# Kernel tuning notes

Hardware: AMD Instinct MI355X
Metric: run time of the kernel (lower is better)

Reference implementation:

```python
import jax, jax.numpy as jnp
import numpy as np

B, L, D = 4, 2048, 1024
H, DK, DV = 16, 64, 64


def setup_inputs() -> dict:
    key = jax.random.key(0)
    ks = jax.random.split(key, 11)
    s = 1.0 / np.sqrt(D)
    so = 1.0 / np.sqrt(H * DV)
    return {
        "query": jax.random.normal(ks[0], (B, L, D), jnp.float32),
        "key": jax.random.normal(ks[1], (B, L, D), jnp.float32),
        "value": jax.random.normal(ks[2], (B, L, D), jnp.float32),
        "W_q": jax.random.uniform(ks[3], (D, H * DK), jnp.float32, -s, s),
        "b_q": jax.random.uniform(ks[4], (H * DK,), jnp.float32, -s, s),
        "W_k": jax.random.uniform(ks[5], (D, H * DK), jnp.float32, -s, s),
        "b_k": jax.random.uniform(ks[6], (H * DK,), jnp.float32, -s, s),
        "W_v": jax.random.uniform(ks[7], (D, H * DV), jnp.float32, -s, s),
        "b_v": jax.random.uniform(ks[8], (H * DV,), jnp.float32, -s, s),
        "W_o": jax.random.uniform(ks[9], (H * DV, D), jnp.float32, -so, so),
        "b_o": jax.random.uniform(ks[10], (D,), jnp.float32, -so, so),
    }


def reference(query, key, value, W_q, b_q, W_k, b_k, W_v, b_v, W_o, b_o):
    # QKV projections, then split heads: [B, L, H*d] -> [B, H, L, d]
    q = (query @ W_q + b_q).reshape(B, L, H, DK).transpose(0, 2, 1, 3)
    k = (key @ W_k + b_k).reshape(B, L, H, DK).transpose(0, 2, 1, 3)
    v = (value @ W_v + b_v).reshape(B, L, H, DV).transpose(0, 2, 1, 3)
    # scaled dot-product attention: softmax(q k^T / sqrt(dk)) v
    scores = jnp.einsum("bhqd,bhkd->bhqk", q, k) / jnp.sqrt(jnp.float32(DK))
    attn = jax.nn.softmax(scores, axis=-1)
    ctx = jnp.einsum("bhqk,bhkd->bhqd", attn, v)
    # combine heads: [B, H, L, dv] -> [B, L, H*dv], output projection
    out = ctx.transpose(0, 2, 1, 3).reshape(B, L, H * DV) @ W_o + b_o
    return out
```

## Files before the change

kernel.cpp:

```cpp
#include <hip/hip_runtime.h>

#define BATCH 4
#define LSEQ 2048
#define DMODEL 1024
#define NHEAD 16
#define DHEAD 64
#define MTOT (BATCH * LSEQ)

typedef _Float16 f16;
typedef _Float16 f16x8 __attribute__((ext_vector_type(8)));
typedef _Float16 f16x4 __attribute__((ext_vector_type(4)));
typedef _Float16 f16x2 __attribute__((ext_vector_type(2)));
typedef float f32x4 __attribute__((ext_vector_type(4)));
typedef float f32x16 __attribute__((ext_vector_type(16)));
typedef unsigned int u32;
typedef unsigned int u32x4 __attribute__((ext_vector_type(4)));

#define SCORE_SCALE 0.180336878f

typedef const __attribute__((address_space(1))) void gvoid;
typedef __attribute__((address_space(3))) void lvoid;
#define GLDS16(g, l) __builtin_amdgcn_global_load_lds((gvoid*)(g), (lvoid*)(l), 16, 0, 0)

#define WAITCNT(s) do { asm volatile("s_waitcnt " s ::: "memory"); \
                        __builtin_amdgcn_sched_barrier(0); } while (0)
#define BAR() __builtin_amdgcn_s_barrier()
#define SCHED0() __builtin_amdgcn_sched_barrier(0)

__global__ __launch_bounds__(256)
void cvt3_f32_f16(const float* __restrict__ in0, const float* __restrict__ in1,
                  const float* __restrict__ in2, f16* __restrict__ out, int n8)
{
    const int y = blockIdx.y;
    const float* in = (y == 0) ? in0 : (y == 1) ? in1 : in2;
    f16* o = out + (size_t)y * (size_t)n8 * 8;
    int i = blockIdx.x * 256 + threadIdx.x;
    if (i >= n8) return;
    float4 a = ((const float4*)in)[2 * i];
    float4 b = ((const float4*)in)[2 * i + 1];
    f16x8 v;
    v[0] = (f16)a.x; v[1] = (f16)a.y; v[2] = (f16)a.z; v[3] = (f16)a.w;
    v[4] = (f16)b.x; v[5] = (f16)b.y; v[6] = (f16)b.z; v[7] = (f16)b.w;
    ((f16x8*)o)[i] = v;
}

__global__ __launch_bounds__(256)
void wconv4(const float* __restrict__ W0, const float* __restrict__ W1,
            const float* __restrict__ W2, const float* __restrict__ W3,
            f16* __restrict__ WtBase)
{
    __shared__ float T[64][68];
    const int z = blockIdx.z;
    const float* W = (z == 0) ? W0 : (z == 1) ? W1 : (z == 2) ? W2 : W3;
    f16* Wt = WtBase + (size_t)z * DMODEL * DMODEL;
    const int t = threadIdx.x;
    const int k0 = blockIdx.y * 64, n0 = blockIdx.x * 64;
    const int tr = t >> 4, tc = (t & 15) * 4;
#pragma unroll
    for (int p = 0; p < 64; p += 16) {
        float4 v = *(const float4*)&W[(size_t)(k0 + tr + p) * DMODEL + n0 + tc];
        *(float4*)&T[tr + p][tc] = v;
    }
    __syncthreads();
    const int n = t >> 2, kc = (t & 3) * 16;
    f16x8 o0, o1;
#pragma unroll
    for (int j = 0; j < 8; ++j) o0[j] = (f16)T[kc + j][n];
#pragma unroll
    for (int j = 0; j < 8; ++j) o1[j] = (f16)T[kc + 8 + j][n];
    *(f16x8*)&Wt[(size_t)(n0 + n) * DMODEL + k0 + kc] = o0;
    *(f16x8*)&Wt[(size_t)(n0 + n) * DMODEL + k0 + kc + 8] = o1;
}

__global__ __launch_bounds__(512, 2)
void gemm_qkv(const f16* __restrict__ A, const f16* __restrict__ Bt,
              const float* __restrict__ b0, const float* __restrict__ b1,
              const float* __restrict__ b2, f16* __restrict__ Cout)
{
    __shared__ f16 As[2][2][128][64];
    __shared__ f16 Bs[2][2][128][64];

    const int t = threadIdx.x;
    const int lane = t & 63;
    const int w = t >> 6, wr = w >> 2, wc = w & 3;
    const int quad = lane >> 4, m16 = lane & 15;
    const int m0 = blockIdx.x * 256, n0 = blockIdx.y * 256;
    const int which = n0 >> 10;

    const int sr = t >> 3;
    const int sc = ((t & 7) << 4) ^ ((sr & 7) << 4);
    const f16* Asrc = A + (size_t)which * MTOT * DMODEL
                        + (size_t)(m0 + sr) * DMODEL + (sc >> 1);
    const f16* Bsrc = Bt + (size_t)(n0 + sr) * DMODEL + (sc >> 1);

    auto stA = [&](int buf, int h, int kt) {
        const f16* s = Asrc + (size_t)(h * 128) * DMODEL + kt * 64;
        GLDS16(s,               &As[buf][h][0][0] + t * 8);
        GLDS16(s + 64 * DMODEL, &As[buf][h][64][0] + t * 8);
    };
    auto stB = [&](int buf, int h, int kt) {
        const f16* s = Bsrc + (size_t)(h * 128) * DMODEL + kt * 64;
        GLDS16(s,               &Bs[buf][h][0][0] + t * 8);
        GLDS16(s + 64 * DMODEL, &Bs[buf][h][64][0] + t * 8);
    };
    auto stageTile = [&](int k) {
        const int b = k & 1;
        stA(b, 0, k); stA(b, 1, k); stB(b, 0, k); stB(b, 1, k);
    };

    const int fsw = (m16 & 7) << 4;
    auto rdA = [&](int buf, int mf, int ks) -> f16x8 {
        return *(const f16x8*)((const char*)&As[buf][wr][0][0]
                               + (mf * 16 + m16) * 128
                               + ((ks * 64 + quad * 16) ^ fsw));
    };
    auto rdB = [&](int buf, int nf, int ks) -> f16x8 {
        return *(const f16x8*)((const char*)&Bs[buf][wc >> 1][0][0]
                               + ((wc & 1) * 64 + nf * 16 + m16) * 128
                               + ((ks * 64 + quad * 16) ^ fsw));
    };

    f32x4 acc[8][4] = {};

    auto compute = [&](int buf) {
        f16x8 af[4][2], bf[4][2];
#pragma unroll
        for (int nf = 0; nf < 4; ++nf)
#pragma unroll
            for (int ks = 0; ks < 2; ++ks)
                bf[nf][ks] = rdB(buf, nf, ks);
#pragma unroll
        for (int mg = 0; mg < 2; ++mg) {
#pragma unroll
            for (int mi = 0; mi < 4; ++mi)
#pragma unroll
                for (int ks = 0; ks < 2; ++ks)
                    af[mi][ks] = rdA(buf, mg * 4 + mi, ks);
#pragma unroll
            for (int mi = 0; mi < 4; ++mi)
#pragma unroll
                for (int ni = 0; ni < 4; ++ni)
#pragma unroll
                    for (int ks = 0; ks < 2; ++ks)
                        acc[mg * 4 + mi][ni] =
                            __builtin_amdgcn_mfma_f32_16x16x32_f16(
                                af[mi][ks], bf[ni][ks],
                                acc[mg * 4 + mi][ni], 0, 0, 0);
        }
    };

    const int NKT = DMODEL / 64;
    stageTile(0);
    stageTile(1);

#pragma unroll 2
    for (int k = 0; k < NKT - 2; ++k) {
        WAITCNT("vmcnt(8)");
        BAR(); SCHED0();
        compute(k & 1);
        WAITCNT("lgkmcnt(0)");
        BAR(); SCHED0();
        stageTile(k + 2);
        SCHED0();
    }
    WAITCNT("vmcnt(8)");
    BAR(); SCHED0();
    compute((NKT - 2) & 1);
    WAITCNT("lgkmcnt(0)");
    BAR(); SCHED0();
    WAITCNT("vmcnt(0)");
    BAR(); SCHED0();
    compute((NKT - 1) & 1);

    const float* bp = (which == 0) ? b0 : (which == 1) ? b1 : b2;
    const float scale = (which == 0) ? SCORE_SCALE : 1.0f;
    f16* o = Cout + (size_t)which * MTOT * DMODEL;
    float bv[4];
    int hh[4], dd[4];
#pragma unroll
    for (int nf = 0; nf < 4; ++nf) {
        const int nn = (n0 + wc * 64 + nf * 16 + m16) & 1023;
        bv[nf] = bp[nn];
        hh[nf] = nn >> 6;
        dd[nf] = nn & 63;
    }
#pragma unroll
    for (int mf = 0; mf < 8; ++mf) {
        const int mrow = m0 + wr * 128 + mf * 16 + quad * 4;
        const int b = mrow >> 11, l0 = mrow & (LSEQ - 1);
        if (which < 2) {
#pragma unroll
            for (int j = 0; j < 4; ++j)
#pragma unroll
                for (int nf = 0; nf < 4; ++nf) {
                    const float v = (acc[mf][nf][j] + bv[nf]) * scale;
                    o[(((size_t)(b * NHEAD + hh[nf]) * LSEQ + l0 + j) << 6)
                      + dd[nf]] = (f16)v;
                }
        } else {
#pragma unroll
            for (int nf = 0; nf < 4; ++nf) {
                f16x4 pk;
#pragma unroll
                for (int j = 0; j < 4; ++j) pk[j] = (f16)(acc[mf][nf][j] + bv[nf]);
                *(f16x4*)&o[(((size_t)(b * NHEAD + hh[nf]) << 6) + dd[nf]) * LSEQ
                            + l0] = pk;
            }
        }
    }
}

__global__ __launch_bounds__(256)
void gemm_f16(const f16* __restrict__ A, const f16* __restrict__ Bt,
              const float* __restrict__ b0, const float* __restrict__ b1,
              const float* __restrict__ b2, void* __restrict__ Cout, int fused)
{
    __shared__ f16 As2[2][128][32];
    __shared__ f16 Bs2[2][128][32];

    const int t = threadIdx.x;
    const int lane = t & 63, w = t >> 6;
    const int quad = lane >> 4, m16 = lane & 15;
    const int m0 = blockIdx.x * 128;
    const int n0 = blockIdx.y * 128;
    const int wm = (w & 1) * 64, wn = (w >> 1) * 64;

    const int which = fused ? (n0 >> 10) : 0;

    f32x4 acc[4][4] = {};

    const f16* Ag = A + (size_t)which * MTOT * DMODEL
                      + (size_t)(m0 + (t >> 2)) * DMODEL + (t & 3) * 8;
    const f16* Bg = Bt + (size_t)(n0 + (t >> 2)) * DMODEL + (t & 3) * 8;
    f16* Al = &As2[0][0][0] + t * 8;
    f16* Bl = &Bs2[0][0][0] + t * 8;

    for (int k0 = 0; k0 < DMODEL; k0 += 64) {
        __syncthreads();
#pragma unroll
        for (int h = 0; h < 2; ++h) {
            GLDS16(Ag + k0 + h * 32, Al + h * 4096);
            GLDS16(Ag + k0 + h * 32 + (size_t)64 * DMODEL, Al + h * 4096 + 2048);
            GLDS16(Bg + k0 + h * 32, Bl + h * 4096);
            GLDS16(Bg + k0 + h * 32 + (size_t)64 * DMODEL, Bl + h * 4096 + 2048);
        }
        __syncthreads();
#pragma unroll
        for (int h = 0; h < 2; ++h) {
            f16x8 af[4], bf[4];
#pragma unroll
            for (int mi = 0; mi < 4; ++mi)
                af[mi] = *(const f16x8*)&As2[h][wm + mi * 16 + m16][quad * 8];
#pragma unroll
            for (int ni = 0; ni < 4; ++ni)
                bf[ni] = *(const f16x8*)&Bs2[h][wn + ni * 16 + m16][quad * 8];
#pragma unroll
            for (int mi = 0; mi < 4; ++mi)
#pragma unroll
                for (int ni = 0; ni < 4; ++ni)
                    acc[mi][ni] = __builtin_amdgcn_mfma_f32_16x16x32_f16(
                        af[mi], bf[ni], acc[mi][ni], 0, 0, 0);
        }
    }

    if (fused) {
        const float* bp = (which == 0) ? b0 : (which == 1) ? b1 : b2;
        const float scale = (which == 0) ? SCORE_SCALE : 1.0f;
        f16* o = (f16*)Cout + (size_t)which * MTOT * DMODEL;
#pragma unroll
        for (int ni = 0; ni < 4; ++ni) {
            const int nn = (n0 + wn + ni * 16 + m16) & 1023;
            const float bv = bp[nn];
            const int h = nn >> 6, d = nn & 63;
#pragma unroll
            for (int mi = 0; mi < 4; ++mi) {
                const int mrow = m0 + wm + mi * 16 + quad * 4;
                const int b = mrow >> 11, l0 = mrow & (LSEQ - 1);
                if (which < 2) {
#pragma unroll
                    for (int j = 0; j < 4; ++j) {
                        const float v = (acc[mi][ni][j] + bv) * scale;
                        o[(((size_t)(b * NHEAD + h) * LSEQ + l0 + j) << 6) + d] = (f16)v;
                    }
                } else {
                    f16x4 pk;
#pragma unroll
                    for (int j = 0; j < 4; ++j) pk[j] = (f16)(acc[mi][ni][j] + bv);
                    *(f16x4*)&o[(((size_t)(b * NHEAD + h) << 6) + d) * LSEQ + l0] = pk;
                }
            }
        }
    } else {
#pragma unroll
        for (int ni = 0; ni < 4; ++ni) {
            const int n = n0 + wn + ni * 16 + m16;
            const float bv = b0[n];
#pragma unroll
            for (int mi = 0; mi < 4; ++mi)
#pragma unroll
                for (int j = 0; j < 4; ++j) {
                    const int m = m0 + wm + mi * 16 + quad * 4 + j;
                    ((float*)Cout)[(size_t)m * DMODEL + n] = acc[mi][ni][j] + bv;
                }
        }
    }
}

__global__ __launch_bounds__(512, 4)
void attn_mfma(const f16* __restrict__ Qh, const f16* __restrict__ Kh,
               const f16* __restrict__ Vt, f16* __restrict__ ctx)
{
    __shared__ f16 Ks[2][64 * 64];
    __shared__ f16 Vs[2][64 * 64];

    const int t = threadIdx.x;
    const int lane = t & 63, w = t >> 6;
    const int l31 = lane & 31;
    const int hi = lane >> 5;
    const int swz = (l31 & 7) << 4;

    const int bid = blockIdx.x;
    const int x = bid & 7, rest = bid >> 3;
    const int qt = rest & 7;
    const int g = x + 8 * (rest >> 3);
    const int q0 = qt * 256 + w * 32;

    const f16* Qg = Qh + (size_t)g * LSEQ * DHEAD;
    const f16* Kg = Kh + (size_t)g * LSEQ * DHEAD;
    const f16* Vg = Vt + (size_t)g * LSEQ * DHEAD;

    f16x8 qf[4];
#pragma unroll
    for (int s = 0; s < 4; ++s)
        qf[s] = *(const f16x8*)&Qg[(size_t)(q0 + l31) * DHEAD + 16 * s + 8 * hi];

    const int srow = t >> 3;
    const int sxs = ((t & 7) << 4) ^ ((srow & 7) << 4);
    const f16* ksrc = Kg + (size_t)srow * DHEAD + (sxs >> 1);
    const f16* vsrc = Vg + (size_t)srow * LSEQ + (sxs >> 1);
    f16* kdst0 = &Ks[0][0] + t * 8;
    f16* vdst0 = &Vs[0][0] + t * 8;
    f16* kdst1 = &Ks[1][0] + t * 8;
    f16* vdst1 = &Vs[1][0] + t * 8;

    f32x16 ctxa[2] = {};
    float lsum = 0.f;

    GLDS16(ksrc, kdst0);
    GLDS16(vsrc, vdst0);
    __syncthreads();

    auto proc = [&](const f32x16& stv, const int kb, const char* Vc) {
        u32 d[8];
#pragma unroll
        for (int r = 0; r < 8; ++r) {
            const float p0 = __builtin_amdgcn_exp2f(stv[2 * r]);
            const float p1 = __builtin_amdgcn_exp2f(stv[2 * r + 1]);
            lsum += p0 + p1;
            f16x2 pk; pk[0] = (f16)p0; pk[1] = (f16)p1;
            d[r] = __builtin_bit_cast(u32, pk);
        }
#pragma unroll
        for (int s = 0; s < 2; ++s) {
            const u32 sendE = hi ? d[4 * s + 0] : d[4 * s + 2];
            const u32 sendO = hi ? d[4 * s + 1] : d[4 * s + 3];
            const u32 recvE = __shfl_xor(sendE, 32);
            const u32 recvO = __shfl_xor(sendO, 32);
            u32x4 paw;
            paw[0] = hi ? recvE : d[4 * s + 0];
            paw[1] = hi ? recvO : d[4 * s + 1];
            paw[2] = hi ? d[4 * s + 2] : recvE;
            paw[3] = hi ? d[4 * s + 3] : recvO;
            const f16x8 pa = __builtin_bit_cast(f16x8, paw);
            const int kbyte = kb * 64 + 32 * s + 16 * hi;
#pragma unroll
            for (int d32 = 0; d32 < 2; ++d32) {
                const int vrow = d32 * 32 + l31;
                const f16x8 vf = *(const f16x8*)(Vc + vrow * 128 + (kbyte ^ swz));
                ctxa[d32] = __builtin_amdgcn_mfma_f32_32x32x16_f16(
                    pa, vf, ctxa[d32], 0, 0, 0);
            }
        }
    };

    auto compute = [&](const f16* Kbuf, const f16* Vbuf) {
        const char* Kc = (const char*)Kbuf;
        const char* Vc = (const char*)Vbuf;
        f32x16 s0 = {}, s1 = {};
#pragma unroll
        for (int s = 0; s < 4; ++s) {
            const int cb = 32 * s + 16 * hi;
            const f16x8 kf0 = *(const f16x8*)(Kc + l31 * 128 + (cb ^ swz));
            const f16x8 kf1 = *(const f16x8*)(Kc + (l31 + 32) * 128 + (cb ^ swz));
            s0 = __builtin_amdgcn_mfma_f32_32x32x16_f16(kf0, qf[s], s0, 0, 0, 0);
            s1 = __builtin_amdgcn_mfma_f32_32x32x16_f16(kf1, qf[s], s1, 0, 0, 0);
        }
        proc(s0, 0, Vc);
        proc(s1, 1, Vc);
    };

    for (int kt = 0; kt < LSEQ; kt += 128) {
        if (kt + 64 < LSEQ) {
            GLDS16(ksrc + (size_t)(kt + 64) * DHEAD, kdst1);
            GLDS16(vsrc + (kt + 64), vdst1);
        }
        compute(&Ks[0][0], &Vs[0][0]);
        __syncthreads();
        if (kt + 128 < LSEQ) {
            GLDS16(ksrc + (size_t)(kt + 128) * DHEAD, kdst0);
            GLDS16(vsrc + (kt + 128), vdst0);
        }
        compute(&Ks[1][0], &Vs[1][0]);
        __syncthreads();
    }

    const float l = lsum + __shfl_xor(lsum, 32);
    const float linv = 1.0f / l;
    const int batch = g >> 4, h = g & 15;
#pragma unroll
    for (int r = 0; r < 16; ++r) {
        const int qr = (r & 3) + 8 * (r >> 2) + 4 * hi;
        const float inv = __shfl(linv, qr);
        f16* op = ctx + ((size_t)(batch * LSEQ + q0 + qr)) * DMODEL
                      + h * 64 + l31;
        op[0]  = (f16)(ctxa[0][r] * inv);
        op[32] = (f16)(ctxa[1][r] * inv);
    }
}

extern "C" void kernel_launch(void* const* d_in, const int* in_sizes, int n_in,
                              void* d_out, int out_size, void* d_ws, size_t ws_size,
                              hipStream_t stream)
{
    const float* query = (const float*)d_in[0];
    const float* key   = (const float*)d_in[1];
    const float* value = (const float*)d_in[2];
    const float* W_q   = (const float*)d_in[3];
    const float* b_q   = (const float*)d_in[4];
    const float* W_k   = (const float*)d_in[5];
    const float* b_k   = (const float*)d_in[6];
    const float* W_v   = (const float*)d_in[7];
    const float* b_v   = (const float*)d_in[8];
    const float* W_o   = (const float*)d_in[9];
    const float* b_o   = (const float*)d_in[10];
    float* out = (float*)d_out;

    const size_t MAT = (size_t)MTOT * DMODEL;
    f16* base = (f16*)d_ws;
    f16* Aq   = base;
    f16* Qhp  = base + 3 * MAT;
    f16* ctxh = base + 6 * MAT;
    f16* Wtq  = base + 7 * MAT;
    f16* Wto  = Wtq + (size_t)3 * DMODEL * DMODEL;

    const int n8 = (int)(MAT / 8);
    cvt3_f32_f16<<<dim3(n8 / 256, 3), 256, 0, stream>>>(query, key, value, Aq, n8);
    wconv4<<<dim3(DMODEL / 64, DMODEL / 64, 4), 256, 0, stream>>>(W_q, W_k, W_v, W_o, Wtq);

    gemm_qkv<<<dim3(MTOT / 256, 3 * DMODEL / 256), 512, 0, stream>>>(
        Aq, Wtq, b_q, b_k, b_v, Qhp);

    attn_mfma<<<BATCH * NHEAD * (LSEQ / 256), 512, 0, stream>>>(
        Qhp, Qhp + MAT, Qhp + 2 * MAT, ctxh);

    gemm_f16<<<dim3(MTOT / 128, DMODEL / 128), 256, 0, stream>>>(
        ctxh, Wto, b_o, nullptr, nullptr, out, 0);
}
```

Baseline: 343.1 us.

## Shrink attention blocks to 256 threads, merge prep kernels, fuse row-sum into fdot2

The two conversion kernels (activation f32->f16 and weight transpose-convert) are merged into one launch that dispatches on blockIdx.y. The attention kernel now uses 256-thread blocks covering 128 queries, doubling the grid, with each thread staging two K/V rows per tile. The softmax row sum is accumulated with a packed fdot2 on the f16-rounded probabilities instead of separate float adds, and the conversion uses cvt_pkrtz. The unused fused path of gemm_f16 is also removed. The smaller blocks should raise scheduling flexibility and cut launch overhead, at the cost of more K/V loads per query and slightly different rounding in the normaliser.

```diff
diff --git a/kernel.cpp b/kernel.cpp
--- a/kernel.cpp
+++ b/kernel.cpp
@@ -10,7 +10,7 @@
 typedef _Float16 f16;
 typedef _Float16 f16x8 __attribute__((ext_vector_type(8)));
 typedef _Float16 f16x4 __attribute__((ext_vector_type(4)));
-typedef _Float16 f16x2 __attribute__((ext_vector_type(2)));
+typedef __fp16 h16x2 __attribute__((ext_vector_type(2)));
 typedef float f32x4 __attribute__((ext_vector_type(4)));
 typedef float f32x16 __attribute__((ext_vector_type(16)));
 typedef unsigned int u32;
@@ -28,33 +28,36 @@
 #define SCHED0() __builtin_amdgcn_sched_barrier(0)
 
 __global__ __launch_bounds__(256)
-void cvt3_f32_f16(const float* __restrict__ in0, const float* __restrict__ in1,
-                  const float* __restrict__ in2, f16* __restrict__ out, int n8)
-{
-    const int y = blockIdx.y;
-    const float* in = (y == 0) ? in0 : (y == 1) ? in1 : in2;
-    f16* o = out + (size_t)y * (size_t)n8 * 8;
-    int i = blockIdx.x * 256 + threadIdx.x;
-    if (i >= n8) return;
-    float4 a = ((const float4*)in)[2 * i];
-    float4 b = ((const float4*)in)[2 * i + 1];
-    f16x8 v;
-    v[0] = (f16)a.x; v[1] = (f16)a.y; v[2] = (f16)a.z; v[3] = (f16)a.w;
-    v[4] = (f16)b.x; v[5] = (f16)b.y; v[6] = (f16)b.z; v[7] = (f16)b.w;
-    ((f16x8*)o)[i] = v;
-}
-
-__global__ __launch_bounds__(256)
-void wconv4(const float* __restrict__ W0, const float* __restrict__ W1,
-            const float* __restrict__ W2, const float* __restrict__ W3,
-            f16* __restrict__ WtBase)
+void prep(const float* __restrict__ in0, const float* __restrict__ in1,
+          const float* __restrict__ in2, f16* __restrict__ out, int n8,
+          const float* __restrict__ W0, const float* __restrict__ W1,
+          const float* __restrict__ W2, const float* __restrict__ W3,
+          f16* __restrict__ WtBase)
 {
     __shared__ float T[64][68];
-    const int z = blockIdx.z;
+    const int t = threadIdx.x;
+    const int y = blockIdx.y;
+
+    if (y < 3) {
+        const float* in = (y == 0) ? in0 : (y == 1) ? in1 : in2;
+        f16* o = out + (size_t)y * (size_t)n8 * 8;
+        int i = blockIdx.x * 256 + t;
+        if (i >= n8) return;
+        float4 a = ((const float4*)in)[2 * i];
+        float4 b = ((const float4*)in)[2 * i + 1];
+        f16x8 v;
+        v[0] = (f16)a.x; v[1] = (f16)a.y; v[2] = (f16)a.z; v[3] = (f16)a.w;
+        v[4] = (f16)b.x; v[5] = (f16)b.y; v[6] = (f16)b.z; v[7] = (f16)b.w;
+        ((f16x8*)o)[i] = v;
+        return;
+    }
+
+    const int id = blockIdx.x;
+    if (id >= 1024) return;
+    const int z = id >> 8, rem = id & 255;
+    const int k0 = (rem >> 4) * 64, n0 = (rem & 15) * 64;
     const float* W = (z == 0) ? W0 : (z == 1) ? W1 : (z == 2) ? W2 : W3;
     f16* Wt = WtBase + (size_t)z * DMODEL * DMODEL;
-    const int t = threadIdx.x;
-    const int k0 = blockIdx.y * 64, n0 = blockIdx.x * 64;
     const int tr = t >> 4, tc = (t & 15) * 4;
 #pragma unroll
     for (int p = 0; p < 64; p += 16) {
@@ -212,8 +215,7 @@
 
 __global__ __launch_bounds__(256)
 void gemm_f16(const f16* __restrict__ A, const f16* __restrict__ Bt,
-              const float* __restrict__ b0, const float* __restrict__ b1,
-              const float* __restrict__ b2, void* __restrict__ Cout, int fused)
+              const float* __restrict__ b0, void* __restrict__ Cout)
 {
     __shared__ f16 As2[2][128][32];
     __shared__ f16 Bs2[2][128][32];
@@ -225,12 +227,9 @@
     const int n0 = blockIdx.y * 128;
     const int wm = (w & 1) * 64, wn = (w >> 1) * 64;
 
-    const int which = fused ? (n0 >> 10) : 0;
-
     f32x4 acc[4][4] = {};
 
-    const f16* Ag = A + (size_t)which * MTOT * DMODEL
-                      + (size_t)(m0 + (t >> 2)) * DMODEL + (t & 3) * 8;
+    const f16* Ag = A + (size_t)(m0 + (t >> 2)) * DMODEL + (t & 3) * 8;
     const f16* Bg = Bt + (size_t)(n0 + (t >> 2)) * DMODEL + (t & 3) * 8;
     f16* Al = &As2[0][0][0] + t * 8;
     f16* Bl = &Bs2[0][0][0] + t * 8;
@@ -263,50 +262,21 @@
         }
     }
 
-    if (fused) {
-        const float* bp = (which == 0) ? b0 : (which == 1) ? b1 : b2;
-        const float scale = (which == 0) ? SCORE_SCALE : 1.0f;
-        f16* o = (f16*)Cout + (size_t)which * MTOT * DMODEL;
-#pragma unroll
-        for (int ni = 0; ni < 4; ++ni) {
-            const int nn = (n0 + wn + ni * 16 + m16) & 1023;
-            const float bv = bp[nn];
-            const int h = nn >> 6, d = nn & 63;
-#pragma unroll
-            for (int mi = 0; mi < 4; ++mi) {
-                const int mrow = m0 + wm + mi * 16 + quad * 4;
-                const int b = mrow >> 11, l0 = mrow & (LSEQ - 1);
-                if (which < 2) {
-#pragma unroll
-                    for (int j = 0; j < 4; ++j) {
-                        const float v = (acc[mi][ni][j] + bv) * scale;
-                        o[(((size_t)(b * NHEAD + h) * LSEQ + l0 + j) << 6) + d] = (f16)v;
-                    }
-                } else {
-                    f16x4 pk;
-#pragma unroll
-                    for (int j = 0; j < 4; ++j) pk[j] = (f16)(acc[mi][ni][j] + bv);
-                    *(f16x4*)&o[(((size_t)(b * NHEAD + h) << 6) + d) * LSEQ + l0] = pk;
-                }
+#pragma unroll
+    for (int ni = 0; ni < 4; ++ni) {
+        const int n = n0 + wn + ni * 16 + m16;
+        const float bv = b0[n];
+#pragma unroll
+        for (int mi = 0; mi < 4; ++mi)
+#pragma unroll
+            for (int j = 0; j < 4; ++j) {
+                const int m = m0 + wm + mi * 16 + quad * 4 + j;
+                ((float*)Cout)[(size_t)m * DMODEL + n] = acc[mi][ni][j] + bv;
             }
-        }
-    } else {
-#pragma unroll
-        for (int ni = 0; ni < 4; ++ni) {
-            const int n = n0 + wn + ni * 16 + m16;
-            const float bv = b0[n];
-#pragma unroll
-            for (int mi = 0; mi < 4; ++mi)
-#pragma unroll
-                for (int j = 0; j < 4; ++j) {
-                    const int m = m0 + wm + mi * 16 + quad * 4 + j;
-                    ((float*)Cout)[(size_t)m * DMODEL + n] = acc[mi][ni][j] + bv;
-                }
-        }
     }
 }
 
-__global__ __launch_bounds__(512, 4)
+__global__ __launch_bounds__(256, 4)
 void attn_mfma(const f16* __restrict__ Qh, const f16* __restrict__ Kh,
                const f16* __restrict__ Vt, f16* __restrict__ ctx)
 {
@@ -321,9 +291,9 @@
 
     const int bid = blockIdx.x;
     const int x = bid & 7, rest = bid >> 3;
-    const int qt = rest & 7;
-    const int g = x + 8 * (rest >> 3);
-    const int q0 = qt * 256 + w * 32;
+    const int qt = rest & 15;
+    const int g = x + 8 * (rest >> 4);
+    const int q0 = qt * 128 + w * 32;
 
     const f16* Qg = Qh + (size_t)g * LSEQ * DHEAD;
     const f16* Kg = Kh + (size_t)g * LSEQ * DHEAD;
@@ -336,28 +306,39 @@
 
     const int srow = t >> 3;
     const int sxs = ((t & 7) << 4) ^ ((srow & 7) << 4);
-    const f16* ksrc = Kg + (size_t)srow * DHEAD + (sxs >> 1);
-    const f16* vsrc = Vg + (size_t)srow * LSEQ + (sxs >> 1);
-    f16* kdst0 = &Ks[0][0] + t * 8;
-    f16* vdst0 = &Vs[0][0] + t * 8;
-    f16* kdst1 = &Ks[1][0] + t * 8;
-    f16* vdst1 = &Vs[1][0] + t * 8;
+    const f16* ksrcA = Kg + (size_t)srow * DHEAD + (sxs >> 1);
+    const f16* vsrcA = Vg + (size_t)srow * LSEQ + (sxs >> 1);
+    const f16* ksrcB = ksrcA + (size_t)32 * DHEAD;
+    const f16* vsrcB = vsrcA + (size_t)32 * LSEQ;
+    f16* kd[2] = {&Ks[0][0] + t * 8, &Ks[1][0] + t * 8};
+    f16* vd[2] = {&Vs[0][0] + t * 8, &Vs[1][0] + t * 8};
+
+    auto stage = [&](int b, int kt) {
+        GLDS16(ksrcA + (size_t)kt * DHEAD, kd[b]);
+        GLDS16(ksrcB + (size_t)kt * DHEAD, kd[b] + 2048);
+        GLDS16(vsrcA + kt, vd[b]);
+        GLDS16(vsrcB + kt, vd[b] + 2048);
+    };
 
     f32x16 ctxa[2] = {};
     float lsum = 0.f;
 
-    GLDS16(ksrc, kdst0);
-    GLDS16(vsrc, vdst0);
+    stage(0, 0);
     __syncthreads();
 
     auto proc = [&](const f32x16& stv, const int kb, const char* Vc) {
         u32 d[8];
+        const h16x2 one2 = {(__fp16)1.0f, (__fp16)1.0f};
 #pragma unroll
         for (int r = 0; r < 8; ++r) {
             const float p0 = __builtin_amdgcn_exp2f(stv[2 * r]);
             const float p1 = __builtin_amdgcn_exp2f(stv[2 * r + 1]);
+            const h16x2 pk = __builtin_amdgcn_cvt_pkrtz(p0, p1);
+#if __has_builtin(__builtin_amdgcn_fdot2)
+            lsum = __builtin_amdgcn_fdot2(pk, one2, lsum, false);
+#else
             lsum += p0 + p1;
-            f16x2 pk; pk[0] = (f16)p0; pk[1] = (f16)p1;
+#endif
             d[r] = __builtin_bit_cast(u32, pk);
         }
 #pragma unroll
@@ -400,16 +381,10 @@
     };
 
     for (int kt = 0; kt < LSEQ; kt += 128) {
-        if (kt + 64 < LSEQ) {
-            GLDS16(ksrc + (size_t)(kt + 64) * DHEAD, kdst1);
-            GLDS16(vsrc + (kt + 64), vdst1);
-        }
+        if (kt + 64 < LSEQ) stage(1, kt + 64);
         compute(&Ks[0][0], &Vs[0][0]);
         __syncthreads();
-        if (kt + 128 < LSEQ) {
-            GLDS16(ksrc + (size_t)(kt + 128) * DHEAD, kdst0);
-            GLDS16(vsrc + (kt + 128), vdst0);
-        }
+        if (kt + 128 < LSEQ) stage(0, kt + 128);
         compute(&Ks[1][0], &Vs[1][0]);
         __syncthreads();
     }
@@ -454,15 +429,15 @@
     f16* Wto  = Wtq + (size_t)3 * DMODEL * DMODEL;
 
     const int n8 = (int)(MAT / 8);
-    cvt3_f32_f16<<<dim3(n8 / 256, 3), 256, 0, stream>>>(query, key, value, Aq, n8);
-    wconv4<<<dim3(DMODEL / 64, DMODEL / 64, 4), 256, 0, stream>>>(W_q, W_k, W_v, W_o, Wtq);
+    prep<<<dim3(n8 / 256, 4), 256, 0, stream>>>(
+        query, key, value, Aq, n8, W_q, W_k, W_v, W_o, Wtq);
 
     gemm_qkv<<<dim3(MTOT / 256, 3 * DMODEL / 256), 512, 0, stream>>>(
         Aq, Wtq, b_q, b_k, b_v, Qhp);
 
-    attn_mfma<<<BATCH * NHEAD * (LSEQ / 256), 512, 0, stream>>>(
+    attn_mfma<<<BATCH * NHEAD * (LSEQ / 128), 256, 0, stream>>>(
         Qhp, Qhp + MAT, Qhp + 2 * MAT, ctxh);
 
     gemm_f16<<<dim3(MTOT / 128, DMODEL / 128), 256, 0, stream>>>(
-        ctxh, Wto, b_o, nullptr, nullptr, out, 0);
+        ctxh, Wto, b_o, out);
 }
```

After: 342.0 us. Within noise of the previous version (-0.3%).
